# Performance work log

Measured on AMD Instinct MI355X. Metric: run time of the kernel, lower is better.

## Reference

```python
import jax, jax.numpy as jnp
import numpy as np

B, G, C = 256, 64, 128          # pictures, groups/picture, curves/group
N = B * G * C                    # 2,097,152 flat curves
EPS = 1e-5


def _bn(x, gamma, beta):
    # torch BatchNorm1d training-mode math: biased variance over batch dim
    mu = x.mean(axis=0)
    var = ((x - mu) ** 2).mean(axis=0)
    return (x - mu) / jnp.sqrt(var + EPS) * gamma + beta


def setup_inputs() -> dict:
    key = jax.random.key(0)
    ks = jax.random.split(key, 16)
    rn = lambda k, s: jax.random.normal(k, s, dtype=jnp.float32) * 0.1
    return {
        "x": jax.random.normal(ks[0], (N, 32), dtype=jnp.float32),
        "dist_mat": jax.random.normal(ks[1], (B, G, 2, 5), dtype=jnp.float32),
        "segment_ids": jnp.arange(N, dtype=jnp.int32) // C,  # curve -> group id
        "w1": rn(ks[2], (24, 32)), "b1": rn(ks[3], (24,)),
        "w2": rn(ks[4], (12, 24)), "b2": rn(ks[5], (12,)),
        "gamma12": jnp.ones((12,), jnp.float32), "beta12": jnp.zeros((12,), jnp.float32),
        "wd": rn(ks[6], (12, 5)), "bd": rn(ks[7], (12,)),
        "gamma36": jnp.ones((36,), jnp.float32), "beta36": jnp.zeros((36,), jnp.float32),
        "wp1": rn(ks[8], (18, 36)), "bp1": rn(ks[9], (18,)),
        "wp2": rn(ks[10], (8, 18)), "bp2": rn(ks[11], (8,)),
        "wp3": rn(ks[12], (2, 8)), "bp3": rn(ks[13], (2,)),
    }


def reference(x, dist_mat, segment_ids, w1, b1, w2, b2, gamma12, beta12,
              wd, bd, gamma36, beta36, wp1, bp1, wp2, bp2, wp3, bp3):
    leaky = jax.nn.leaky_relu  # slope 0.01, same as nn.LeakyReLU default
    # per-curve MLP: 32 -> 24 -> 12, then BatchNorm over all curves
    h = leaky(x @ w1.T + b1)               # [N, 24]
    h = leaky(h @ w2.T + b2)               # [N, 12]
    h = _bn(h, gamma12, beta12)            # [N, 12]
    # ragged segment-mean: curves -> groups (uniform segments of size C)
    groups = jax.ops.segment_sum(h, segment_ids, num_segments=B * G) / C
    groups = groups.reshape(B, G, 12)      # groups_layer1 per picture
    # distance adaptation: dist_mat[:, :, 0, :] -> Linear(5,12) -> leaky
    cor = leaky(jnp.einsum('bgk,dk->bgd', dist_mat[:, :, 0, :], wd) + bd)  # [B,G,12]
    # three pooling levels (distance-weighted elementwise-multiply reduce)
    L1 = groups.mean(axis=1)               # [B, 12]
    g2 = cor * groups
    L2 = g2.mean(axis=1)
    g3 = cor * g2
    L3 = g3.mean(axis=1)
    sum_pic = jnp.concatenate([L1, L2, L3], axis=1)  # [B, 36]
    s = _bn(sum_pic, gamma36, beta36)
    p1 = leaky(s @ wp1.T + bp1)            # [B, 18]
    p2 = leaky(p1 @ wp2.T + bp2)           # [B, 8]  (pred_level2)
    p3 = jax.nn.softmax(p2 @ wp3.T + bp3, axis=1)  # [B, 2] (pred_level3)
    return (p2, p3)
```

## Files before the change

kernel.cpp:

```cpp
#include <hip/hip_runtime.h>
#include <hip/hip_bf16.h>

#define N_CURVES 2097152
#define NG       16384
#define B_PIC    256
#define G_PER_B  64
#define NSLOT    64

__device__ __forceinline__ float leaky(float v) {
    return fmaxf(v, 0.01f * v);
}

__global__ __launch_bounds__(256) void kA(const float* __restrict__ x,
                                          const float* __restrict__ w1,
                                          const float* __restrict__ b1,
                                          const float* __restrict__ w2,
                                          const float* __restrict__ b2,
                                          float* __restrict__ partials,
                                          float* __restrict__ groupSums)
{
    const int tid = threadIdx.x;
    const size_t curve = (size_t)blockIdx.x * 256 + tid;

    float xr[32];
    const float4* xv = (const float4*)(x + curve * 32);
#pragma unroll
    for (int i = 0; i < 8; ++i) {
        float4 v = xv[i];
        xr[4 * i + 0] = v.x; xr[4 * i + 1] = v.y;
        xr[4 * i + 2] = v.z; xr[4 * i + 3] = v.w;
    }

    float h1[24];
#pragma unroll
    for (int j = 0; j < 24; ++j) {
        float acc = b1[j];
#pragma unroll
        for (int k = 0; k < 32; ++k) acc = fmaf(xr[k], w1[j * 32 + k], acc);
        h1[j] = leaky(acc);
    }

    float h2[12];
#pragma unroll
    for (int j = 0; j < 12; ++j) {
        float acc = b2[j];
#pragma unroll
        for (int k = 0; k < 24; ++k) acc = fmaf(h1[k], w2[j * 24 + k], acc);
        h2[j] = leaky(acc);
    }

    __shared__ float wsum[4][12];
    __shared__ float wsq[4][12];
    const int lane = tid & 63, wid = tid >> 6;
#pragma unroll
    for (int c = 0; c < 12; ++c) {
        float v = h2[c];
        float q = v * v;
#pragma unroll
        for (int off = 32; off >= 1; off >>= 1) {
            v += __shfl_down(v, off);
            q += __shfl_down(q, off);
        }
        if (lane == 0) { wsum[wid][c] = v; wsq[wid][c] = q; }
    }
    __syncthreads();

    if (tid < 12) {
        const int c = tid;
        const float g0 = wsum[0][c] + wsum[1][c];
        const float g1 = wsum[2][c] + wsum[3][c];
        groupSums[(size_t)(2 * blockIdx.x) * 12 + c]     = g0;
        groupSums[(size_t)(2 * blockIdx.x + 1) * 12 + c] = g1;
        const int slot = blockIdx.x & (NSLOT - 1);
        atomicAdd(&partials[slot * 24 + c], g0 + g1);
        const float q = wsq[0][c] + wsq[1][c] + wsq[2][c] + wsq[3][c];
        atomicAdd(&partials[slot * 24 + 12 + c], q);
    }
}

__global__ __launch_bounds__(64) void kB(const float* __restrict__ partials,
                                         const float* __restrict__ groupSums,
                                         const float* __restrict__ dist,
                                         const float* __restrict__ wd,
                                         const float* __restrict__ bd,
                                         const float* __restrict__ gamma12,
                                         const float* __restrict__ beta12,
                                         float* __restrict__ sum_pic)
{
    __shared__ float scale[12], shift[12];
    const int g = threadIdx.x;
    const int b = blockIdx.x;

    if (g < 12) {
        float S = 0.f, Q = 0.f;
        for (int s = 0; s < NSLOT; ++s) {
            S += partials[s * 24 + g];
            Q += partials[s * 24 + 12 + g];
        }
        const float mu  = S * (1.0f / (float)N_CURVES);
        const float var = Q * (1.0f / (float)N_CURVES) - mu * mu;
        const float inv = rsqrtf(var + 1e-5f);
        scale[g] = inv * gamma12[g];
        shift[g] = beta12[g] - mu * inv * gamma12[g];
    }
    __syncthreads();

    const float* dm = dist + (size_t)(b * G_PER_B + g) * 2 * 5;
    const float d0 = dm[0], d1 = dm[1], d2 = dm[2], d3 = dm[3], d4 = dm[4];
    const float* gs = groupSums + (size_t)(b * G_PER_B + g) * 12;

    float a1[12], a2[12], a3[12];
#pragma unroll
    for (int d = 0; d < 12; ++d) {
        float cor = bd[d];
        cor = fmaf(d0, wd[d * 5 + 0], cor);
        cor = fmaf(d1, wd[d * 5 + 1], cor);
        cor = fmaf(d2, wd[d * 5 + 2], cor);
        cor = fmaf(d3, wd[d * 5 + 3], cor);
        cor = fmaf(d4, wd[d * 5 + 4], cor);
        cor = leaky(cor);
        float t = gs[d] * (1.0f / 128.0f);
        t = t * scale[d] + shift[d];
        a1[d] = t;
        a2[d] = cor * t;
        a3[d] = cor * cor * t;
    }

#pragma unroll
    for (int d = 0; d < 12; ++d) {
        float v1 = a1[d], v2 = a2[d], v3 = a3[d];
#pragma unroll
        for (int off = 32; off >= 1; off >>= 1) {
            v1 += __shfl_down(v1, off);
            v2 += __shfl_down(v2, off);
            v3 += __shfl_down(v3, off);
        }
        if (g == 0) {
            sum_pic[b * 36 + d]      = v1 * (1.0f / 64.0f);
            sum_pic[b * 36 + 12 + d] = v2 * (1.0f / 64.0f);
            sum_pic[b * 36 + 24 + d] = v3 * (1.0f / 64.0f);
        }
    }
}

__global__ __launch_bounds__(256) void kC(const float* __restrict__ sum_pic,
                                          const float* __restrict__ gamma36,
                                          const float* __restrict__ beta36,
                                          const float* __restrict__ wp1,
                                          const float* __restrict__ bp1,
                                          const float* __restrict__ wp2,
                                          const float* __restrict__ bp2,
                                          const float* __restrict__ wp3,
                                          const float* __restrict__ bp3,
                                          float* __restrict__ out)
{
    const int t = threadIdx.x;
    float s[36];
#pragma unroll
    for (int c = 0; c < 36; ++c) s[c] = sum_pic[t * 36 + c];

    __shared__ float mu[36], inv[36];
    __shared__ float wred[4], wred2[4];
    const int lane = t & 63, wid = t >> 6;

    for (int c = 0; c < 36; ++c) {
        float v = s[c];
        float q = v * v;
#pragma unroll
        for (int off = 32; off >= 1; off >>= 1) {
            v += __shfl_down(v, off);
            q += __shfl_down(q, off);
        }
        if (lane == 0) { wred[wid] = v; wred2[wid] = q; }
        __syncthreads();
        if (t == 0) {
            const float S = wred[0] + wred[1] + wred[2] + wred[3];
            const float Q = wred2[0] + wred2[1] + wred2[2] + wred2[3];
            const float m = S * (1.0f / 256.0f);
            mu[c]  = m;
            inv[c] = rsqrtf(Q * (1.0f / 256.0f) - m * m + 1e-5f);
        }
        __syncthreads();
    }

#pragma unroll
    for (int c = 0; c < 36; ++c)
        s[c] = (s[c] - mu[c]) * inv[c] * gamma36[c] + beta36[c];

    float p1[18];
#pragma unroll
    for (int j = 0; j < 18; ++j) {
        float acc = bp1[j];
#pragma unroll
        for (int k = 0; k < 36; ++k) acc = fmaf(s[k], wp1[j * 36 + k], acc);
        p1[j] = leaky(acc);
    }
    float p2[8];
#pragma unroll
    for (int j = 0; j < 8; ++j) {
        float acc = bp2[j];
#pragma unroll
        for (int k = 0; k < 18; ++k) acc = fmaf(p1[k], wp2[j * 18 + k], acc);
        p2[j] = leaky(acc);
    }
    float l0 = bp3[0], l1 = bp3[1];
#pragma unroll
    for (int k = 0; k < 8; ++k) {
        l0 = fmaf(p2[k], wp3[k], l0);
        l1 = fmaf(p2[k], wp3[8 + k], l1);
    }
    const float m  = fmaxf(l0, l1);
    const float e0 = __expf(l0 - m);
    const float e1 = __expf(l1 - m);
    const float rd = 1.0f / (e0 + e1);

#pragma unroll
    for (int j = 0; j < 8; ++j) out[t * 8 + j] = p2[j];
    out[2048 + t * 2 + 0] = e0 * rd;
    out[2048 + t * 2 + 1] = e1 * rd;
}

extern "C" void kernel_launch(void* const* d_in, const int* in_sizes, int n_in,
                              void* d_out, int out_size, void* d_ws, size_t ws_size,
                              hipStream_t stream) {
    const float* x       = (const float*)d_in[0];
    const float* dist    = (const float*)d_in[1];
    const float* w1      = (const float*)d_in[3];
    const float* b1      = (const float*)d_in[4];
    const float* w2      = (const float*)d_in[5];
    const float* b2      = (const float*)d_in[6];
    const float* gamma12 = (const float*)d_in[7];
    const float* beta12  = (const float*)d_in[8];
    const float* wd      = (const float*)d_in[9];
    const float* bd      = (const float*)d_in[10];
    const float* gamma36 = (const float*)d_in[11];
    const float* beta36  = (const float*)d_in[12];
    const float* wp1     = (const float*)d_in[13];
    const float* bp1     = (const float*)d_in[14];
    const float* wp2     = (const float*)d_in[15];
    const float* bp2     = (const float*)d_in[16];
    const float* wp3     = (const float*)d_in[17];
    const float* bp3     = (const float*)d_in[18];

    float* ws        = (float*)d_ws;
    float* partials  = ws;
    float* groupSums = ws + NSLOT * 24;
    float* sum_pic   = groupSums + (size_t)NG * 12;

    hipMemsetAsync(partials, 0, NSLOT * 24 * sizeof(float), stream);

    kA<<<N_CURVES / 256, 256, 0, stream>>>(x, w1, b1, w2, b2, partials, groupSums);
    kB<<<B_PIC, G_PER_B, 0, stream>>>(partials, groupSums, dist, wd, bd,
                                      gamma12, beta12, sum_pic);
    kC<<<1, 256, 0, stream>>>(sum_pic, gamma36, beta36,
                              wp1, bp1, wp2, bp2, wp3, bp3, (float*)d_out);
}
```

Before: 476.9 us.

## Stage x through swizzled shared memory with coalesced loads; simplify final batchnorm reduction

New measurement: 445.0 us. 1.07x faster.

```diff
diff --git a/kernel.cpp b/kernel.cpp
--- a/kernel.cpp
+++ b/kernel.cpp
@@ -11,24 +11,38 @@
     return fmaxf(v, 0.01f * v);
 }
 
-__global__ __launch_bounds__(256) void kA(const float* __restrict__ x,
-                                          const float* __restrict__ w1,
-                                          const float* __restrict__ b1,
-                                          const float* __restrict__ w2,
-                                          const float* __restrict__ b2,
-                                          float* __restrict__ partials,
-                                          float* __restrict__ groupSums)
+__global__ __launch_bounds__(256, 4) void kA(const float* __restrict__ x,
+                                             const float* __restrict__ w1,
+                                             const float* __restrict__ b1,
+                                             const float* __restrict__ w2,
+                                             const float* __restrict__ b2,
+                                             float* __restrict__ partials,
+                                             float* __restrict__ groupSums)
 {
+    __shared__ float4 xs[256 * 8];
+    __shared__ float wsum[4][12];
+    __shared__ float wsq[4][12];
+
     const int tid = threadIdx.x;
-    const size_t curve = (size_t)blockIdx.x * 256 + tid;
+    const size_t blockBase = (size_t)blockIdx.x * 2048;
+
+    const float4* __restrict__ xg = (const float4*)x;
+#pragma unroll
+    for (int i = 0; i < 8; ++i) {
+        const int idx = i * 256 + tid;
+        const float4 v = xg[blockBase + idx];
+        const int c = idx >> 3;
+        const int j = idx & 7;
+        xs[c * 8 + (j ^ (c & 7))] = v;
+    }
+    __syncthreads();
 
     float xr[32];
-    const float4* xv = (const float4*)(x + curve * 32);
-#pragma unroll
-    for (int i = 0; i < 8; ++i) {
-        float4 v = xv[i];
-        xr[4 * i + 0] = v.x; xr[4 * i + 1] = v.y;
-        xr[4 * i + 2] = v.z; xr[4 * i + 3] = v.w;
+#pragma unroll
+    for (int j = 0; j < 8; ++j) {
+        const float4 v = xs[tid * 8 + (j ^ (tid & 7))];
+        xr[4 * j + 0] = v.x; xr[4 * j + 1] = v.y;
+        xr[4 * j + 2] = v.z; xr[4 * j + 3] = v.w;
     }
 
     float h1[24];
@@ -49,8 +63,6 @@
         h2[j] = leaky(acc);
     }
 
-    __shared__ float wsum[4][12];
-    __shared__ float wsq[4][12];
     const int lane = tid & 63, wid = tid >> 6;
 #pragma unroll
     for (int c = 0; c < 12; ++c) {
@@ -155,37 +167,34 @@
                                           float* __restrict__ out)
 {
     const int t = threadIdx.x;
+    __shared__ float sm[256 * 37];
+    __shared__ float scale[36], shift[36];
+
     float s[36];
 #pragma unroll
-    for (int c = 0; c < 36; ++c) s[c] = sum_pic[t * 36 + c];
-
-    __shared__ float mu[36], inv[36];
-    __shared__ float wred[4], wred2[4];
-    const int lane = t & 63, wid = t >> 6;
-
     for (int c = 0; c < 36; ++c) {
-        float v = s[c];
-        float q = v * v;
-#pragma unroll
-        for (int off = 32; off >= 1; off >>= 1) {
-            v += __shfl_down(v, off);
-            q += __shfl_down(q, off);
-        }
-        if (lane == 0) { wred[wid] = v; wred2[wid] = q; }
-        __syncthreads();
-        if (t == 0) {
-            const float S = wred[0] + wred[1] + wred[2] + wred[3];
-            const float Q = wred2[0] + wred2[1] + wred2[2] + wred2[3];
-            const float m = S * (1.0f / 256.0f);
-            mu[c]  = m;
-            inv[c] = rsqrtf(Q * (1.0f / 256.0f) - m * m + 1e-5f);
-        }
-        __syncthreads();
-    }
+        s[c] = sum_pic[t * 36 + c];
+        sm[t * 37 + c] = s[c];
+    }
+    __syncthreads();
+
+    if (t < 36) {
+        float S = 0.f, Q = 0.f;
+        for (int i = 0; i < 256; ++i) {
+            const float v = sm[i * 37 + t];
+            S += v;
+            Q += v * v;
+        }
+        const float m   = S * (1.0f / 256.0f);
+        const float inv = rsqrtf(Q * (1.0f / 256.0f) - m * m + 1e-5f);
+        scale[t] = inv * gamma36[t];
+        shift[t] = beta36[t] - m * inv * gamma36[t];
+    }
+    __syncthreads();
 
 #pragma unroll
     for (int c = 0; c < 36; ++c)
-        s[c] = (s[c] - mu[c]) * inv[c] * gamma36[c] + beta36[c];
+        s[c] = s[c] * scale[c] + shift[c];
 
     float p1[18];
 #pragma unroll
```
